# Kernel optimization log

Hardware: AMD Instinct MI355X
Metric: run time of the kernel (lower is better)

## Reference

```python
import jax, jax.numpy as jnp
import numpy as np
from jax import lax

SCORE_THRESHOLD = 0.01
NMS_THRESHOLD = 0.5
MAX_DETECTIONS = 100
PRE_NMS_TOPK = 512  # fixed-shape candidate pool per class (tf NMS is unbounded; 512 >> max_detections covers it)
NEG_INF = -jnp.inf


def setup_inputs() -> dict:
    key = jax.random.key(0)
    k1, k2, k3, k4, k5 = jax.random.split(key, 5)
    B, N, C = 32, 50000, 10
    # valid (x1,y1,x2,y2) boxes: random top-left + positive width/height
    xy = jax.random.uniform(k1, (B, N, 2), dtype=jnp.float32) * 500.0
    wh = jax.random.uniform(k2, (B, N, 2), dtype=jnp.float32) * 100.0 + 1.0
    boxes = jnp.concatenate([xy, xy + wh], axis=-1)
    classification = jax.random.uniform(k3, (B, N, C), dtype=jnp.float32)
    rotation = jax.random.normal(k4, (B, N, 3), dtype=jnp.float32)
    translation = jax.random.normal(k5, (B, N, 3), dtype=jnp.float32)
    return {"boxes": boxes, "classification": classification,
            "rotation": rotation, "translation": translation}


def _iou_matrix(b):  # b: (K,4) in (x1,y1,x2,y2)
    x1, y1, x2, y2 = b[:, 0], b[:, 1], b[:, 2], b[:, 3]
    area = (x2 - x1) * (y2 - y1)  # (K,)
    ix1 = jnp.maximum(x1[:, None], x1[None, :])
    iy1 = jnp.maximum(y1[:, None], y1[None, :])
    ix2 = jnp.minimum(x2[:, None], x2[None, :])
    iy2 = jnp.minimum(y2[:, None], y2[None, :])
    inter = jnp.maximum(ix2 - ix1, 0.0) * jnp.maximum(iy2 - iy1, 0.0)
    union = area[:, None] + area[None, :] - inter
    return jnp.where(union > 0.0, inter / union, 0.0)  # (K,K)


def _greedy_nms_keep(iou, valid):
    # iou: (K,K) for boxes already sorted by descending score; valid: (K,) bool
    K = iou.shape[0]
    def body(suppressed, xs):
        iou_row, valid_i, i = xs
        keep_i = valid_i & jnp.logical_not(suppressed[i])
        suppressed = jnp.where(keep_i, suppressed | (iou_row > NMS_THRESHOLD), suppressed)
        return suppressed, keep_i
    _, keep = lax.scan(body, jnp.zeros((K,), bool), (iou, valid, jnp.arange(K)))
    return keep


def _per_class(scores, boxes_i):
    # scores: (N,), boxes_i: (N,4) -> kept candidate scores (K,) (-inf where dropped) and anchor idx (K,)
    sc = jnp.where(scores > SCORE_THRESHOLD, scores, NEG_INF)
    vals, idx = lax.top_k(sc, PRE_NMS_TOPK)          # sorted desc
    valid = vals > SCORE_THRESHOLD                    # also false for -inf pads
    iou = _iou_matrix(boxes_i[idx])
    keep = _greedy_nms_keep(iou, valid)
    keep = keep & (jnp.cumsum(keep.astype(jnp.int32)) <= MAX_DETECTIONS)
    return jnp.where(keep, vals, NEG_INF), idx


def _per_image(boxes_i, cls_i, rot_i, trans_i):
    # boxes_i (N,4), cls_i (N,C), rot_i (N,3), trans_i (N,3)
    C = cls_i.shape[1]
    sc_ck, idx_ck = jax.vmap(_per_class, in_axes=(1, None))(cls_i, boxes_i)  # (C,K)
    labels_ck = jnp.broadcast_to(jnp.arange(C, dtype=jnp.int32)[:, None], sc_ck.shape)
    sc_flat = sc_ck.reshape(-1)
    idx_flat = idx_ck.reshape(-1)
    lab_flat = labels_ck.reshape(-1)
    top_scores, sel = lax.top_k(sc_flat, MAX_DETECTIONS)   # global top-k across classes
    sel_idx = idx_flat[sel]
    sel_lab = lab_flat[sel]
    valid = jnp.isfinite(top_scores)
    out_boxes = jnp.where(valid[:, None], boxes_i[sel_idx], -1.0)
    out_scores = jnp.where(valid, top_scores, -1.0)
    out_labels = jnp.where(valid, sel_lab, -1).astype(jnp.int32)
    out_rot = jnp.where(valid[:, None], rot_i[sel_idx], -1.0)
    out_trans = jnp.where(valid[:, None], trans_i[sel_idx], -1.0)
    return out_boxes, out_scores, out_labels, out_rot, out_trans


def reference(boxes, classification, rotation, translation):
    return jax.vmap(_per_image)(boxes, classification, rotation, translation)
```

## Files before the change

### kernel.cpp

```cpp
#include <hip/hip_runtime.h>
#include <math.h>

typedef unsigned int u32;
typedef unsigned long long u64;

constexpr int NB   = 32;
constexpr int NN   = 50000;
constexpr int NC   = 10;
constexpr int KK   = 512;
constexpr int MAXD = 100;
constexpr int CAP  = 2048;
constexpr int LCAP = 192;
constexpr int GCH  = 2500;
constexpr int KMAX = 1024;
constexpr u32 TBIN = 252;

constexpr int OFF_BOX = 0;
constexpr int OFF_SC  = NB * MAXD * 4;
constexpr int OFF_LB  = OFF_SC + NB * MAXD;
constexpr int OFF_RT  = OFF_LB + NB * MAXD;
constexpr int OFF_TR  = OFF_RT + NB * MAXD * 3;

__device__ __forceinline__ u32 ord_f32(float s) {
  u32 u = __float_as_uint(s);
  return (u & 0x80000000u) ? ~u : (u | 0x80000000u);
}
__device__ __forceinline__ float unord_f32(u32 o) {
  u32 u = (o & 0x80000000u) ? (o & 0x7FFFFFFFu) : ~o;
  return __uint_as_float(u);
}
__device__ __forceinline__ u64 make_key(float s, u32 i) {
  float sp = (s > 0.01f) ? s : -INFINITY;
  return ((u64)ord_f32(sp) << 32) | (u64)(u32)(~i);
}
__device__ __forceinline__ u32 digest16(float x) {
  if (!(x > 0.01f)) return 0;
  u32 q = (u32)(x * 65536.0f);
  return q > 65535u ? 65535u : q;
}
__device__ __forceinline__ float readlane_f(float v, int lane) {
  return __int_as_float(__builtin_amdgcn_readlane(__float_as_int(v), lane));
}
__device__ __forceinline__ u64 readlane_u64(u64 v, int lane) {
  u32 lo = __builtin_amdgcn_readlane((u32)v, lane);
  u32 hi = __builtin_amdgcn_readlane((u32)(v >> 32), lane);
  return ((u64)hi << 32) | lo;
}
__device__ __forceinline__ int clamp_idx(int idx) {
  return idx < 0 ? 0 : (idx >= NN ? NN - 1 : idx);
}

__global__ __launch_bounds__(512) void gather_kernel(
    const float* __restrict__ cls, u64* __restrict__ glist,
    u32* __restrict__ gcnt) {
  const int blk = blockIdx.x;
  const int b = blk / 20, ch = blk % 20;
  const float* src = cls + (size_t)b * NN * NC + (size_t)ch * GCH * NC;
  __shared__ u32 lcnt[NC];
  __shared__ u32 lbase[NC];
  __shared__ u64 lbuf[NC][LCAP];
  const int t = threadIdx.x;
  if (t < NC) lcnt[t] = 0;
  __syncthreads();
  for (int q = t; q < GCH * NC / 4; q += 512) {
    float4 v = ((const float4*)src)[q];
    float arr[4] = {v.x, v.y, v.z, v.w};
#pragma unroll
    for (int k = 0; k < 4; ++k) {
      int e = q * 4 + k;
      int c = e % 10;
      float x = arr[k];
      if ((digest16(x) >> 8) >= TBIN) {
        u32 idx = (u32)((ch * (GCH * NC) + e) / 10);
        u32 p = atomicAdd(&lcnt[c], 1u);
        if (p < (u32)LCAP) {
          lbuf[c][p] = make_key(x, idx);
        } else {
          u32 g = atomicAdd(&gcnt[b * NC + c], 1u);
          if (g < (u32)CAP) glist[(size_t)(b * NC + c) * CAP + g] = make_key(x, idx);
        }
      }
    }
  }
  __syncthreads();
  if (t < NC) {
    u32 n = min(lcnt[t], (u32)LCAP);
    lbase[t] = atomicAdd(&gcnt[b * NC + t], n);
  }
  __syncthreads();
  for (int c = 0; c < NC; ++c) {
    u32 n = min(lcnt[c], (u32)LCAP);
    u32 base = lbase[c];
    for (u32 i = t; i < n; i += 512) {
      u32 p = base + i;
      if (p < (u32)CAP) glist[(size_t)(b * NC + c) * CAP + p] = lbuf[c][i];
    }
  }
}

__global__ __launch_bounds__(512) void selnms_kernel(
    const float* __restrict__ cls, const u64* __restrict__ glist,
    const u32* __restrict__ gcnt, const float* __restrict__ boxes,
    int* __restrict__ tidx, float* __restrict__ ksc) {
  __shared__ __align__(16) unsigned char smem[32768 + 4096 + 8192 + 2048 + 64];
  u64* cand = (u64*)smem;
  ushort (*prank)[8] = (ushort(*)[8])(smem + 8192);
  u64 (*rowm)[8] = (u64(*)[8])smem;
  u64* sel = (u64*)(smem + 32768);
  float4* bx4 = (float4*)(smem + 36864);
  float* ars = (float*)(smem + 45056);
  u64* kmask = (u64*)(smem + 47104);
  __shared__ int s_cnt, s_d;

  const int bc = blockIdx.x;
  const int b = bc / NC;
  const int t = threadIdx.x;
  const int lane = t & 63, wv = t >> 6;

  int M = (int)gcnt[bc];
  if (M >= KK && M <= KMAX) {
    for (int i = t; i < KMAX; i += 512)
      cand[i] = (i < M) ? glist[(size_t)bc * CAP + i] : (u64)i;
  } else {
    const int c = bc % NC;
    const float* sbase = cls + (size_t)b * NN * NC + c;
    u32* hist = (u32*)prank;
    for (int i = t; i < 4096; i += 512) hist[i] = 0;
    if (t == 0) s_cnt = 0;
    __syncthreads();
    for (int i = t; i < NN; i += 512)
      atomicAdd(&hist[digest16(sbase[(size_t)i * NC]) >> 4], 1u);
    __syncthreads();
    if (t == 0) {
      u32 run = 0, d = 1;
      for (int i = 4095; i >= 1; --i) {
        run += hist[i];
        if (run >= (u32)KK) { d = (u32)i; break; }
        d = 1;
      }
      s_d = (int)d;
    }
    __syncthreads();
    const u32 dstar = (u32)s_d;
    for (int i = t; i < KMAX; i += 512) cand[i] = (u64)i;
    __syncthreads();
    for (int i = t; i < NN; i += 512) {
      float x = sbase[(size_t)i * NC];
      u32 dg = digest16(x) >> 4;
      if (dg >= dstar && dg >= 1) {
        int p = atomicAdd(&s_cnt, 1);
        if (p < KMAX) cand[p] = make_key(x, (u32)i);
      }
    }
    __syncthreads();
    M = min(s_cnt, KMAX);
  }
  sel[t] = make_key(-INFINITY, 0);
  __syncthreads();

  {
    u64 myk[16];
#pragma unroll
    for (int k = 0; k < 16; ++k) myk[k] = cand[lane + k * 64];
    int rnk[16];
#pragma unroll
    for (int k = 0; k < 16; ++k) rnk[k] = 0;
    const int j0 = wv * 128;
    for (int jj = 0; jj < 64; ++jj) {
      const ulonglong2 v = *(const ulonglong2*)&cand[j0 + jj * 2];
#pragma unroll
      for (int k = 0; k < 16; ++k) {
        rnk[k] += (v.x > myk[k]) ? 1 : 0;
        rnk[k] += (v.y > myk[k]) ? 1 : 0;
      }
    }
#pragma unroll
    for (int k = 0; k < 16; ++k) prank[lane + k * 64][wv] = (ushort)rnk[k];
  }
  __syncthreads();
#pragma unroll
  for (int h = 0; h < 2; ++h) {
    const int i = h * 512 + t;
    const uint4 pv = *(const uint4*)&prank[i][0];
    const int r = (int)(pv.x & 0xFFFFu) + (int)(pv.x >> 16) +
                  (int)(pv.y & 0xFFFFu) + (int)(pv.y >> 16) +
                  (int)(pv.z & 0xFFFFu) + (int)(pv.z >> 16) +
                  (int)(pv.w & 0xFFFFu) + (int)(pv.w >> 16);
    if (i < M && r < KK) sel[r] = cand[i];
  }
  __syncthreads();

  {
    const u64 k = sel[t];
    const int idx = clamp_idx((int)(~(u32)k));
    tidx[bc * KK + t] = idx;
    const float4 bx = *(const float4*)(boxes + ((size_t)b * NN + idx) * 4);
    bx4[t] = bx;
    ars[t] = (bx.z - bx.x) * (bx.w - bx.y);
  }
  __syncthreads();

  float jx1[8], jy1[8], jx2[8], jy2[8], jar[8];
#pragma unroll
  for (int q = 0; q < 8; ++q) {
    const float4 bb = bx4[q * 64 + lane];
    jx1[q] = bb.x; jy1[q] = bb.y; jx2[q] = bb.z; jy2[q] = bb.w;
    jar[q] = ars[q * 64 + lane];
  }
  __syncthreads();


#pragma unroll
  for (int g = 0; g < 8; ++g) {
    for (int rr = 0; rr < 8; ++rr) {
      const int il = wv + 8 * rr;
      const int i = g * 64 + il;
      const float bix1 = readlane_f(jx1[g], il);
      const float biy1 = readlane_f(jy1[g], il);
      const float bix2 = readlane_f(jx2[g], il);
      const float biy2 = readlane_f(jy2[g], il);
      const float bia  = readlane_f(jar[g], il);
      u64 m[8];
#pragma unroll
      for (int q = 0; q < 8; ++q) {
        m[q] = 0;
        if (q >= g) {
          float ix1 = fmaxf(bix1, jx1[q]);
          float iy1 = fmaxf(biy1, jy1[q]);
          float ix2 = fminf(bix2, jx2[q]);
          float iy2 = fminf(biy2, jy2[q]);
          float iw = fmaxf(ix2 - ix1, 0.0f);
          float ih = fmaxf(iy2 - iy1, 0.0f);
          float inter = iw * ih;
          float uni = bia + jar[q] - inter;
          bool s = (uni > 0.0f) && ((inter - 0.5f * uni) > uni * 0x1p-25f);
          m[q] = __ballot(s);
        }
      }
      u64 word = m[0];
#pragma unroll
      for (int q = 1; q < 8; ++q) word = (lane == q) ? m[q] : word;
      if (lane < 8) rowm[i][lane] = word;
    }
  }
  __syncthreads();

  if (wv == 0) {
    u64 vw_[8], kw[8];
#pragma unroll
    for (int q = 0; q < 8; ++q) {
      const float sc = unord_f32((u32)(sel[q * 64 + lane] >> 32));
      vw_[q] = __ballot(sc > 0.01f);
      kw[q] = 0;
    }
    u64 vsup = 0;
    int count = 0;
    bool done = false;
#pragma unroll
    for (int w = 0; w < 8; ++w) {
      if (!done) {
        u64 av = vw_[w] & ~readlane_u64(vsup, w);
        while (av) {
          const int bbit = (int)__builtin_ctzll(av);
          const int i = w * 64 + bbit;
          kw[w] |= 1ull << bbit;
          if (++count == MAXD) { done = true; break; }
          const u64 row = (lane < 8) ? rowm[i][lane] : 0;
          vsup |= row;
          const u64 mask_gt = (bbit == 63) ? 0ull : (~0ull << (bbit + 1));
          av = vw_[w] & ~readlane_u64(vsup, w) & mask_gt;
        }
      }
    }
    if (lane < 8) {
      u64 word = kw[0];
#pragma unroll
      for (int q = 1; q < 8; ++q) word = (lane == q) ? kw[q] : word;
      kmask[lane] = word;
    }
  }
  __syncthreads();
  {
    const float sc = unord_f32((u32)(sel[t] >> 32));
    const bool keep = (kmask[t >> 6] >> (t & 63)) & 1ull;
    ksc[(size_t)bc * KK + t] = keep ? sc : -INFINITY;
  }
}

__global__ __launch_bounds__(512) void final_kernel(
    const float* __restrict__ boxes, const float* __restrict__ rot,
    const float* __restrict__ trans, const int* __restrict__ tidx,
    const float* __restrict__ ksc, float* __restrict__ out) {
  const int b = blockIdx.x;
  __shared__ __align__(16) u64 ck[KMAX];
  __shared__ __align__(16) ushort prank[KMAX][8];
  __shared__ u64 top[MAXD];
  __shared__ int cnt;
  const int t = threadIdx.x;
  const int lane = t & 63, wv = t >> 6;
  if (t == 0) cnt = 0;
  if (t < MAXD) top[t] = make_key(-INFINITY, 0);
  for (int i = t; i < KMAX; i += 512) ck[i] = (u64)i;
  __syncthreads();
  for (int j = t; j < NC * KK; j += 512) {
    float s = ksc[b * NC * KK + j];
    if (s != -INFINITY) {
      int p = atomicAdd(&cnt, 1);
      if (p < KMAX) ck[p] = ((u64)ord_f32(s) << 32) | (u64)(u32)(~(u32)j);
    }
  }
  __syncthreads();
  const int n = min(cnt, KMAX);
  {
    u64 myk[16];
#pragma unroll
    for (int k = 0; k < 16; ++k) myk[k] = ck[lane + k * 64];
    int rnk[16];
#pragma unroll
    for (int k = 0; k < 16; ++k) rnk[k] = 0;
    const int j0 = wv * 128;
    for (int jj = 0; jj < 64; ++jj) {
      const ulonglong2 v = *(const ulonglong2*)&ck[j0 + jj * 2];
#pragma unroll
      for (int k = 0; k < 16; ++k) {
        rnk[k] += (v.x > myk[k]) ? 1 : 0;
        rnk[k] += (v.y > myk[k]) ? 1 : 0;
      }
    }
#pragma unroll
    for (int k = 0; k < 16; ++k) prank[lane + k * 64][wv] = (ushort)rnk[k];
  }
  __syncthreads();
#pragma unroll
  for (int h = 0; h < 2; ++h) {
    const int i = h * 512 + t;
    const uint4 pv = *(const uint4*)&prank[i][0];
    const int r = (int)(pv.x & 0xFFFFu) + (int)(pv.x >> 16) +
                  (int)(pv.y & 0xFFFFu) + (int)(pv.y >> 16) +
                  (int)(pv.z & 0xFFFFu) + (int)(pv.z >> 16) +
                  (int)(pv.w & 0xFFFFu) + (int)(pv.w >> 16);
    if (i < n && r < MAXD) top[r] = ck[i];
  }
  __syncthreads();

  if (t < MAXD) {
    float b0 = -1.f, b1 = -1.f, b2 = -1.f, b3 = -1.f;
    float os = -1.f, ol = -1.f;
    float r0 = -1.f, r1 = -1.f, r2 = -1.f;
    float t0 = -1.f, t1 = -1.f, t2 = -1.f;
    const u64 k = top[t];
    const float sc = unord_f32((u32)(k >> 32));
    if (sc != -INFINITY) {
      int j = (int)(~(u32)k);
      int c = j >> 9, slot = j & (KK - 1);
      int idx = tidx[(b * NC + c) * KK + slot];
      os = sc;
      ol = (float)c;
      const float4 bx = *(const float4*)(boxes + ((size_t)b * NN + idx) * 4);
      b0 = bx.x; b1 = bx.y; b2 = bx.z; b3 = bx.w;
      const float* rp = rot + ((size_t)b * NN + idx) * 3;
      r0 = rp[0]; r1 = rp[1]; r2 = rp[2];
      const float* tp = trans + ((size_t)b * NN + idx) * 3;
      t0 = tp[0]; t1 = tp[1]; t2 = tp[2];
    }
    const int o = b * MAXD + t;
    out[OFF_BOX + (size_t)o * 4 + 0] = b0;
    out[OFF_BOX + (size_t)o * 4 + 1] = b1;
    out[OFF_BOX + (size_t)o * 4 + 2] = b2;
    out[OFF_BOX + (size_t)o * 4 + 3] = b3;
    out[OFF_SC + o] = os;
    out[OFF_LB + o] = ol;
    out[OFF_RT + (size_t)o * 3 + 0] = r0;
    out[OFF_RT + (size_t)o * 3 + 1] = r1;
    out[OFF_RT + (size_t)o * 3 + 2] = r2;
    out[OFF_TR + (size_t)o * 3 + 0] = t0;
    out[OFF_TR + (size_t)o * 3 + 1] = t1;
    out[OFF_TR + (size_t)o * 3 + 2] = t2;
  }
}

extern "C" void kernel_launch(void* const* d_in, const int* in_sizes, int n_in,
                              void* d_out, int out_size, void* d_ws, size_t ws_size,
                              hipStream_t stream) {
  const float* boxes = (const float*)d_in[0];
  const float* cls   = (const float*)d_in[1];
  const float* rot   = (const float*)d_in[2];
  const float* trans = (const float*)d_in[3];
  float* out = (float*)d_out;

  u64* glist = (u64*)d_ws;
  int* tidx  = (int*)(glist + (size_t)NB * NC * CAP);
  float* ksc = (float*)(tidx + NB * NC * KK);
  u32* gcnt  = (u32*)(ksc + NB * NC * KK);

  hipMemsetAsync(gcnt, 0, NB * NC * sizeof(u32), stream);
  gather_kernel<<<NB * 20, 512, 0, stream>>>(cls, glist, gcnt);
  selnms_kernel<<<NB * NC, 512, 0, stream>>>(cls, glist, gcnt, boxes, tidx, ksc);
  final_kernel<<<NB, 512, 0, stream>>>(boxes, rot, trans, tidx, ksc, out);
}
```

Before: 135.5 us.

## Limit precomputed IoU mask rows and compute later rows lazily during NMS

```diff
diff --git a/kernel.cpp b/kernel.cpp
--- a/kernel.cpp
+++ b/kernel.cpp
@@ -14,6 +14,7 @@
 constexpr int GCH  = 2500;
 constexpr int KMAX = 1024;
 constexpr u32 TBIN = 252;
+constexpr int RLIM = 192;
 
 constexpr int OFF_BOX = 0;
 constexpr int OFF_SC  = NB * MAXD * 4;
@@ -102,14 +103,14 @@
     const float* __restrict__ cls, const u64* __restrict__ glist,
     const u32* __restrict__ gcnt, const float* __restrict__ boxes,
     int* __restrict__ tidx, float* __restrict__ ksc) {
-  __shared__ __align__(16) unsigned char smem[32768 + 4096 + 8192 + 2048 + 64];
+  __shared__ __align__(16) unsigned char smem[28736];
   u64* cand = (u64*)smem;
   ushort (*prank)[8] = (ushort(*)[8])(smem + 8192);
+  u64* sel = (u64*)(smem + 24576);
+  u64* kmask = (u64*)(smem + 28672);
   u64 (*rowm)[8] = (u64(*)[8])smem;
-  u64* sel = (u64*)(smem + 32768);
-  float4* bx4 = (float4*)(smem + 36864);
-  float* ars = (float*)(smem + 45056);
-  u64* kmask = (u64*)(smem + 47104);
+  float4* bx4 = (float4*)(smem + 12288);
+  float* ars = (float*)(smem + 20480);
   __shared__ int s_cnt, s_d;
 
   const int bc = blockIdx.x;
@@ -166,7 +167,9 @@
 #pragma unroll
     for (int k = 0; k < 16; ++k) rnk[k] = 0;
     const int j0 = wv * 128;
-    for (int jj = 0; jj < 64; ++jj) {
+    const int rem = M - j0;
+    const int jjmax = rem <= 0 ? 0 : (rem >= 128 ? 64 : ((rem + 1) >> 1));
+    for (int jj = 0; jj < jjmax; ++jj) {
       const ulonglong2 v = *(const ulonglong2*)&cand[j0 + jj * 2];
 #pragma unroll
       for (int k = 0; k < 16; ++k) {
@@ -211,7 +214,7 @@
 
 
 #pragma unroll
-  for (int g = 0; g < 8; ++g) {
+  for (int g = 0; g < RLIM / 64; ++g) {
     for (int rr = 0; rr < 8; ++rr) {
       const int il = wv + 8 * rr;
       const int i = g * 64 + il;
@@ -265,8 +268,37 @@
           const int i = w * 64 + bbit;
           kw[w] |= 1ull << bbit;
           if (++count == MAXD) { done = true; break; }
-          const u64 row = (lane < 8) ? rowm[i][lane] : 0;
-          vsup |= row;
+          if (w < RLIM / 64) {
+            const u64 row = (lane < 8) ? rowm[i][lane] : 0;
+            vsup |= row;
+          } else {
+            const float bix1 = readlane_f(jx1[w], bbit);
+            const float biy1 = readlane_f(jy1[w], bbit);
+            const float bix2 = readlane_f(jx2[w], bbit);
+            const float biy2 = readlane_f(jy2[w], bbit);
+            const float bia  = readlane_f(jar[w], bbit);
+            u64 m[8];
+#pragma unroll
+            for (int q = 0; q < 8; ++q) {
+              m[q] = 0;
+              if (q >= w) {
+                float ix1 = fmaxf(bix1, jx1[q]);
+                float iy1 = fmaxf(biy1, jy1[q]);
+                float ix2 = fminf(bix2, jx2[q]);
+                float iy2 = fminf(biy2, jy2[q]);
+                float iw = fmaxf(ix2 - ix1, 0.0f);
+                float ih = fmaxf(iy2 - iy1, 0.0f);
+                float inter = iw * ih;
+                float uni = bia + jar[q] - inter;
+                bool s = (uni > 0.0f) && ((inter - 0.5f * uni) > uni * 0x1p-25f);
+                m[q] = __ballot(s);
+              }
+            }
+            u64 word = m[0];
+#pragma unroll
+            for (int q = 1; q < 8; ++q) word = (lane == q) ? m[q] : word;
+            vsup |= word;
+          }
           const u64 mask_gt = (bbit == 63) ? 0ull : (~0ull << (bbit + 1));
           av = vw_[w] & ~readlane_u64(vsup, w) & mask_gt;
         }
@@ -319,7 +351,9 @@
 #pragma unroll
     for (int k = 0; k < 16; ++k) rnk[k] = 0;
     const int j0 = wv * 128;
-    for (int jj = 0; jj < 64; ++jj) {
+    const int rem = n - j0;
+    const int jjmax = rem <= 0 ? 0 : (rem >= 128 ? 64 : ((rem + 1) >> 1));
+    for (int jj = 0; jj < jjmax; ++jj) {
       const ulonglong2 v = *(const ulonglong2*)&ck[j0 + jj * 2];
 #pragma unroll
       for (int k = 0; k < 16; ++k) {
```

Measured after the change: 115.6 us. 14.7% less time.
